# Optimization experiments

Hardware: AMD Instinct MI355X
Metric: run time of the kernel (lower is better)

Reference implementation:

```python
import jax, jax.numpy as jnp
import numpy as np


def soft_thresholding(x, a):
    # sh(x, a) = max(0, |x| - a) * sign(x) == relu(x - a) - relu(-x - a)
    return jax.nn.relu(x - a) - jax.nn.relu(-x - a)


def setup_inputs() -> dict:
    key = jax.random.key(0)
    kA, kb = jax.random.split(key)
    bs, m, n = 32, 256, 512
    A = jax.random.normal(kA, (bs, m, n), dtype=jnp.float32)
    b = jax.random.normal(kb, (bs, m), dtype=jnp.float32)
    return {"A": A, "b": b, "bs": bs, "iters": 1000}


def reference(A, b, bs, iters, alpha=0.02, beta=0.02):
    # A: (bs, m, n), b: (bs, m). PDHG iteration:
    #   x = sh(x - alpha * A^T u, alpha)
    m, n = A.shape[1], A.shape[2]
    x0 = jnp.zeros((bs, n), dtype=jnp.float32)
    u0 = jnp.zeros((bs, m), dtype=jnp.float32)

    def step(carry, _):
        x, u = carry
        x_new = soft_thresholding(x - alpha * jnp.einsum('bmn,bm->bn', A, u), alpha)
        u_new = u + beta * (jnp.einsum('bmn,bn->bm', A, 2.0 * x_new - x) - b)
        return (x_new, u_new), None

    (x, u), _ = jax.lax.scan(step, (x0, u0), None, length=iters)
    return x
```

## Files before the change

### kernel.cpp

```cpp
#include <hip/hip_runtime.h>

#define BS    32
#define MDIM  256
#define NDIM  512
#define ITERS 1000
#define WPB   4
#define RPW   128
#define BLK   512
#define ALPHA 0.02f
#define BETA  0.02f

#define ATS        516
#define ATILE_FL   (32 * ATS)
#define WBUF_OFF   ATILE_FL
#define WBLK       20
#define P_OFF      (WBUF_OFF + 32 * WBLK)
#define C_OFF      (P_OFF + RPW * 32)
#define BT_OFF     (C_OFF + RPW)
#define SMEM_FL    (BT_OFF + 32)

#define SLAB_FL   (2 * BS * NDIM)

__device__ __forceinline__ unsigned ld_coh_u32(const void* p) {
  return __hip_atomic_load(reinterpret_cast<const unsigned*>(p),
                           __ATOMIC_RELAXED, __HIP_MEMORY_SCOPE_AGENT);
}
__device__ __forceinline__ void st_coh_u32(void* p, unsigned v) {
  __hip_atomic_store(reinterpret_cast<unsigned*>(p), v,
                     __ATOMIC_RELAXED, __HIP_MEMORY_SCOPE_AGENT);
}
__device__ __forceinline__ unsigned tagf(float v, unsigned tag) {
  return (__float_as_uint(v) & ~0xFFu) | tag;
}

__global__ __launch_bounds__(BLK, 1) void pdhg_kernel(
    const float* __restrict__ A, const float* __restrict__ Bvec,
    float* __restrict__ out, float* __restrict__ slab)
{
  __shared__ float smem[SMEM_FL];
  const int tid   = threadIdx.x;
  const int bid   = blockIdx.x;
  const int batch = bid & (BS - 1);
  const int slice = bid >> 5;
  const int i0    = slice * RPW;

  const int tj = tid & 31;
  const int ti = tid >> 5;

  float acc[8][16];
#pragma unroll
  for (int r = 0; r < 8; ++r)
#pragma unroll
    for (int s = 0; s < 16; ++s) acc[r][s] = 0.f;
  float cacc[8];
#pragma unroll
  for (int r = 0; r < 8; ++r) cacc[r] = 0.f;

  const float* Ag = A + (size_t)batch * MDIM * NDIM;

  for (int mt = 0; mt < MDIM / 32; ++mt) {
#pragma unroll 4
    for (int q = 0; q < 8; ++q) {
      int f  = q * 512 + tid;
      int mm = f >> 7;
      int j  = (f & 127) << 2;
      float4 v = *reinterpret_cast<const float4*>(
          Ag + (size_t)(mt * 32 + mm) * NDIM + j);
      *reinterpret_cast<float4*>(
          &smem[(j >> 4) * ATS + mm * 16 + (j & 15)]) = v;
    }
    if (tid < 32) smem[BT_OFF + tid] = Bvec[batch * MDIM + mt * 32 + tid];
    __syncthreads();

    const int ibase = ((i0 + 8 * ti) >> 4) * ATS + ((8 * ti) & 15);
    const int jbase = tj * ATS;
    for (int mm = 0; mm < 32; ++mm) {
      float4 a0 = *reinterpret_cast<const float4*>(&smem[ibase + mm * 16]);
      float4 a1 = *reinterpret_cast<const float4*>(&smem[ibase + mm * 16 + 4]);
      float ai[8] = {a0.x, a0.y, a0.z, a0.w, a1.x, a1.y, a1.z, a1.w};
      float aj[16];
#pragma unroll
      for (int kk = 0; kk < 4; ++kk) {
        float4 v = *reinterpret_cast<const float4*>(
            &smem[jbase + mm * 16 + 4 * kk]);
        aj[4*kk] = v.x; aj[4*kk+1] = v.y; aj[4*kk+2] = v.z; aj[4*kk+3] = v.w;
      }
#pragma unroll
      for (int r = 0; r < 8; ++r)
#pragma unroll
        for (int s = 0; s < 16; ++s) acc[r][s] = fmaf(ai[r], aj[s], acc[r][s]);
      if (tj == 0) {
        float bv = smem[BT_OFF + mm];
#pragma unroll
        for (int r = 0; r < 8; ++r) cacc[r] = fmaf(ai[r], bv, cacc[r]);
      }
    }
    __syncthreads();
  }
  if (tj == 0) {
#pragma unroll
    for (int r = 0; r < 8; ++r) smem[C_OFF + ti * 8 + r] = cacc[r];
  }
  __syncthreads();

  const bool owner   = (tid & 3) == 0;
  const int  i_own   = tid >> 2;
  const float c_reg  = smem[C_OFF + i_own];
  float x = 0.f, t = 0.f;

  float* myslot = slab + batch * NDIM + i0 + i_own;
  const float* myrd = slab + batch * NDIM + tid;

  for (int k = 0; k < ITERS; ++k) {
    float xn = 0.f;
    if (owner) {
      float y = x - ALPHA * t;
      xn = fmaxf(y - ALPHA, 0.f) - fmaxf(-y - ALPHA, 0.f);
    }
    if (k == ITERS - 1) { x = xn; break; }

    const int par = (k & 1) * BS * NDIM;
    const unsigned tag = (unsigned)(k + 1) & 0xFFu;
    if (owner) {
      float wv = 2.f * xn - x;
      x = xn;
      st_coh_u32(myslot + par, tagf(wv, tag));
    }

    unsigned qq;
    do {
      qq = ld_coh_u32(myrd + par);
    } while ((qq ^ tag) & 0xFFu);

    smem[WBUF_OFF + (tid >> 4) * WBLK + (tid & 15)] = __uint_as_float(qq);
    __syncthreads();

    float wv[16];
    {
      const float* wb = &smem[WBUF_OFF + tj * WBLK];
#pragma unroll
      for (int kk = 0; kk < 4; ++kk) {
        float4 v = *reinterpret_cast<const float4*>(wb + 4 * kk);
        wv[4*kk] = v.x; wv[4*kk+1] = v.y; wv[4*kk+2] = v.z; wv[4*kk+3] = v.w;
      }
    }
#pragma unroll
    for (int r = 0; r < 8; ++r) {
      float p = 0.f;
#pragma unroll
      for (int s = 0; s < 16; ++s) p = fmaf(acc[r][s], wv[s], p);
      smem[P_OFF + (ti * 8 + r) * 32 + tj] = p;
    }
    __syncthreads();

    {
      int ired = tid >> 2, prt = tid & 3;
      const float* pp = &smem[P_OFF + ired * 32 + prt * 8];
      float4 pa = *reinterpret_cast<const float4*>(pp);
      float4 pb = *reinterpret_cast<const float4*>(pp + 4);
      float s8 = (pa.x + pa.y) + (pa.z + pa.w) +
                 (pb.x + pb.y) + (pb.z + pb.w);
      s8 += __shfl_xor(s8, 1);
      s8 += __shfl_xor(s8, 2);
      if (owner) t += BETA * (s8 - c_reg);
    }
  }

  if (owner) out[(size_t)batch * NDIM + i0 + i_own] = x;
}

extern "C" void kernel_launch(void* const* d_in, const int* in_sizes, int n_in,
                              void* d_out, int out_size, void* d_ws, size_t ws_size,
                              hipStream_t stream) {
  const float* A = (const float*)d_in[0];
  const float* b = (const float*)d_in[1];
  float* out  = (float*)d_out;
  float* slab = (float*)d_ws;

  hipMemsetAsync(d_ws, 0, SLAB_FL * sizeof(float), stream);

  void* args[] = {(void*)&A, (void*)&b, (void*)&out, (void*)&slab};
  hipLaunchCooperativeKernel((const void*)pdhg_kernel, dim3(BS * WPB), dim3(BLK),
                             args, 0, stream);
}
```

Measured before the change: 1.542 ms.

## Remap Gram matvec per-wavefront to drop block barriers from iteration loop

Each wavefront now owns 16 output rows across all 512 columns, keeping a 16x8 Gram slice per lane. Each lane polls 8 slab entries directly, and a transpose-style shuffle reduction across the wavefront replaces the LDS staging buffers and both __syncthreads in the per-iteration loop. The aim is to remove intra-block barrier and LDS round-trip latency from the 1000 serial iterations. In exchange, every lane issues 8 coherent polling loads per iteration and the reduction needs more shuffles. The launch-bounds hint is also relaxed to 2 blocks per SM.

```diff
diff --git a/kernel.cpp b/kernel.cpp
--- a/kernel.cpp
+++ b/kernel.cpp
@@ -5,21 +5,15 @@
 #define NDIM  512
 #define ITERS 1000
 #define WPB   4
-#define RPW   128
 #define BLK   512
 #define ALPHA 0.02f
 #define BETA  0.02f
 
-#define ATS        516
-#define ATILE_FL   (32 * ATS)
-#define WBUF_OFF   ATILE_FL
-#define WBLK       20
-#define P_OFF      (WBUF_OFF + 32 * WBLK)
-#define C_OFF      (P_OFF + RPW * 32)
-#define BT_OFF     (C_OFF + RPW)
-#define SMEM_FL    (BT_OFF + 32)
+#define ATS      520
+#define BT_OFF   (32 * ATS)
+#define SMEM_FL  (BT_OFF + 32)
 
-#define SLAB_FL   (2 * BS * NDIM)
+#define SLAB_FL  (2 * BS * NDIM)
 
 __device__ __forceinline__ unsigned ld_coh_u32(const void* p) {
   return __hip_atomic_load(reinterpret_cast<const unsigned*>(p),
@@ -33,7 +27,7 @@
   return (__float_as_uint(v) & ~0xFFu) | tag;
 }
 
-__global__ __launch_bounds__(BLK, 1) void pdhg_kernel(
+__global__ __launch_bounds__(BLK, 2) void pdhg_kernel(
     const float* __restrict__ A, const float* __restrict__ Bvec,
     float* __restrict__ out, float* __restrict__ slab)
 {
@@ -42,19 +36,19 @@
   const int bid   = blockIdx.x;
   const int batch = bid & (BS - 1);
   const int slice = bid >> 5;
-  const int i0    = slice * RPW;
+  const int lane  = tid & 63;
+  const int widx  = tid >> 6;
+  const int rowbase = slice * 128 + widx * 16;
+  const int row_own = lane & 15;
+  const int i_own   = rowbase + row_own;
+  const int c0      = lane * 8;
 
-  const int tj = tid & 31;
-  const int ti = tid >> 5;
-
-  float acc[8][16];
+  float acc[16][8];
 #pragma unroll
-  for (int r = 0; r < 8; ++r)
+  for (int r = 0; r < 16; ++r)
 #pragma unroll
-    for (int s = 0; s < 16; ++s) acc[r][s] = 0.f;
-  float cacc[8];
-#pragma unroll
-  for (int r = 0; r < 8; ++r) cacc[r] = 0.f;
+    for (int c = 0; c < 8; ++c) acc[r][c] = 0.f;
+  float cacc = 0.f;
 
   const float* Ag = A + (size_t)batch * MDIM * NDIM;
 
@@ -66,107 +60,108 @@
       int j  = (f & 127) << 2;
       float4 v = *reinterpret_cast<const float4*>(
           Ag + (size_t)(mt * 32 + mm) * NDIM + j);
-      *reinterpret_cast<float4*>(
-          &smem[(j >> 4) * ATS + mm * 16 + (j & 15)]) = v;
+      *reinterpret_cast<float4*>(&smem[mm * ATS + j]) = v;
     }
     if (tid < 32) smem[BT_OFF + tid] = Bvec[batch * MDIM + mt * 32 + tid];
     __syncthreads();
 
-    const int ibase = ((i0 + 8 * ti) >> 4) * ATS + ((8 * ti) & 15);
-    const int jbase = tj * ATS;
-    for (int mm = 0; mm < 32; ++mm) {
-      float4 a0 = *reinterpret_cast<const float4*>(&smem[ibase + mm * 16]);
-      float4 a1 = *reinterpret_cast<const float4*>(&smem[ibase + mm * 16 + 4]);
-      float ai[8] = {a0.x, a0.y, a0.z, a0.w, a1.x, a1.y, a1.z, a1.w};
-      float aj[16];
+#pragma unroll 2
+    for (int m = 0; m < 32; ++m) {
+      const float* row = &smem[m * ATS];
+      float4 a0 = *reinterpret_cast<const float4*>(row + rowbase);
+      float4 a1 = *reinterpret_cast<const float4*>(row + rowbase + 4);
+      float4 a2 = *reinterpret_cast<const float4*>(row + rowbase + 8);
+      float4 a3 = *reinterpret_cast<const float4*>(row + rowbase + 12);
+      float ai[16] = {a0.x,a0.y,a0.z,a0.w, a1.x,a1.y,a1.z,a1.w,
+                      a2.x,a2.y,a2.z,a2.w, a3.x,a3.y,a3.z,a3.w};
+      float4 j0 = *reinterpret_cast<const float4*>(row + c0);
+      float4 j1 = *reinterpret_cast<const float4*>(row + c0 + 4);
+      float aj[8] = {j0.x,j0.y,j0.z,j0.w, j1.x,j1.y,j1.z,j1.w};
+      float bm  = smem[BT_OFF + m];
+      float aio = row[i_own];
 #pragma unroll
-      for (int kk = 0; kk < 4; ++kk) {
-        float4 v = *reinterpret_cast<const float4*>(
-            &smem[jbase + mm * 16 + 4 * kk]);
-        aj[4*kk] = v.x; aj[4*kk+1] = v.y; aj[4*kk+2] = v.z; aj[4*kk+3] = v.w;
-      }
+      for (int r = 0; r < 16; ++r)
 #pragma unroll
-      for (int r = 0; r < 8; ++r)
-#pragma unroll
-        for (int s = 0; s < 16; ++s) acc[r][s] = fmaf(ai[r], aj[s], acc[r][s]);
-      if (tj == 0) {
-        float bv = smem[BT_OFF + mm];
-#pragma unroll
-        for (int r = 0; r < 8; ++r) cacc[r] = fmaf(ai[r], bv, cacc[r]);
-      }
+        for (int c = 0; c < 8; ++c) acc[r][c] = fmaf(ai[r], aj[c], acc[r][c]);
+      cacc = fmaf(aio, bm, cacc);
     }
     __syncthreads();
   }
-  if (tj == 0) {
-#pragma unroll
-    for (int r = 0; r < 8; ++r) smem[C_OFF + ti * 8 + r] = cacc[r];
-  }
-  __syncthreads();
 
-  const bool owner   = (tid & 3) == 0;
-  const int  i_own   = tid >> 2;
-  const float c_reg  = smem[C_OFF + i_own];
   float x = 0.f, t = 0.f;
-
-  float* myslot = slab + batch * NDIM + i0 + i_own;
-  const float* myrd = slab + batch * NDIM + tid;
+  float*       myslot = slab + batch * NDIM + i_own;
+  const float* myrd   = slab + batch * NDIM + c0;
 
   for (int k = 0; k < ITERS; ++k) {
-    float xn = 0.f;
-    if (owner) {
-      float y = x - ALPHA * t;
-      xn = fmaxf(y - ALPHA, 0.f) - fmaxf(-y - ALPHA, 0.f);
-    }
+    float y  = x - ALPHA * t;
+    float xn = fmaxf(y - ALPHA, 0.f) - fmaxf(-y - ALPHA, 0.f);
     if (k == ITERS - 1) { x = xn; break; }
 
-    const int par = (k & 1) * BS * NDIM;
+    const int      par = (k & 1) * BS * NDIM;
     const unsigned tag = (unsigned)(k + 1) & 0xFFu;
-    if (owner) {
-      float wv = 2.f * xn - x;
-      x = xn;
-      st_coh_u32(myslot + par, tagf(wv, tag));
+    float wv = 2.f * xn - x;
+    x = xn;
+    if (lane < 16) st_coh_u32(myslot + par, tagf(wv, tag));
+
+    unsigned q[8];
+    unsigned bad;
+    do {
+      bad = 0u;
+#pragma unroll
+      for (int j = 0; j < 8; ++j) {
+        q[j] = ld_coh_u32(myrd + par + j);
+        bad |= (q[j] ^ tag);
+      }
+    } while (bad & 0xFFu);
+
+    float wr[8];
+#pragma unroll
+    for (int j = 0; j < 8; ++j) wr[j] = __uint_as_float(q[j]);
+
+    float S[16];
+#pragma unroll
+    for (int r = 0; r < 16; ++r) {
+      float p = acc[r][0] * wr[0];
+#pragma unroll
+      for (int c = 1; c < 8; ++c) p = fmaf(acc[r][c], wr[c], p);
+      S[r] = p;
     }
 
-    unsigned qq;
-    do {
-      qq = ld_coh_u32(myrd + par);
-    } while ((qq ^ tag) & 0xFFu);
+    const bool b0 = (lane & 1), b1 = (lane & 2), b2 = (lane & 4), b3 = (lane & 8);
+    float T[8];
+#pragma unroll
+    for (int i = 0; i < 8; ++i) {
+      float keep = b0 ? S[2*i+1] : S[2*i];
+      float send = b0 ? S[2*i]   : S[2*i+1];
+      T[i] = keep + __shfl_xor(send, 1);
+    }
+    float U[4];
+#pragma unroll
+    for (int i = 0; i < 4; ++i) {
+      float keep = b1 ? T[2*i+1] : T[2*i];
+      float send = b1 ? T[2*i]   : T[2*i+1];
+      U[i] = keep + __shfl_xor(send, 2);
+    }
+    float V[2];
+#pragma unroll
+    for (int i = 0; i < 2; ++i) {
+      float keep = b2 ? U[2*i+1] : U[2*i];
+      float send = b2 ? U[2*i]   : U[2*i+1];
+      V[i] = keep + __shfl_xor(send, 4);
+    }
+    float Wv;
+    {
+      float keep = b3 ? V[1] : V[0];
+      float send = b3 ? V[0] : V[1];
+      Wv = keep + __shfl_xor(send, 8);
+    }
+    Wv += __shfl_xor(Wv, 16);
+    Wv += __shfl_xor(Wv, 32);
 
-    smem[WBUF_OFF + (tid >> 4) * WBLK + (tid & 15)] = __uint_as_float(qq);
-    __syncthreads();
-
-    float wv[16];
-    {
-      const float* wb = &smem[WBUF_OFF + tj * WBLK];
-#pragma unroll
-      for (int kk = 0; kk < 4; ++kk) {
-        float4 v = *reinterpret_cast<const float4*>(wb + 4 * kk);
-        wv[4*kk] = v.x; wv[4*kk+1] = v.y; wv[4*kk+2] = v.z; wv[4*kk+3] = v.w;
-      }
-    }
-#pragma unroll
-    for (int r = 0; r < 8; ++r) {
-      float p = 0.f;
-#pragma unroll
-      for (int s = 0; s < 16; ++s) p = fmaf(acc[r][s], wv[s], p);
-      smem[P_OFF + (ti * 8 + r) * 32 + tj] = p;
-    }
-    __syncthreads();
-
-    {
-      int ired = tid >> 2, prt = tid & 3;
-      const float* pp = &smem[P_OFF + ired * 32 + prt * 8];
-      float4 pa = *reinterpret_cast<const float4*>(pp);
-      float4 pb = *reinterpret_cast<const float4*>(pp + 4);
-      float s8 = (pa.x + pa.y) + (pa.z + pa.w) +
-                 (pb.x + pb.y) + (pb.z + pb.w);
-      s8 += __shfl_xor(s8, 1);
-      s8 += __shfl_xor(s8, 2);
-      if (owner) t += BETA * (s8 - c_reg);
-    }
+    t += BETA * (Wv - cacc);
   }
 
-  if (owner) out[(size_t)batch * NDIM + i0 + i_own] = x;
+  if (lane < 16) out[(size_t)batch * NDIM + i_own] = x;
 }
 
 extern "C" void kernel_launch(void* const* d_in, const int* in_sizes, int n_in,
```

Measured after the change: 5.387 ms. 249% more time.
